# Kernel optimization log

Measured on AMD Instinct MI355X. Metric: run time of the kernel, lower is better.

## Reference

```python
import jax, jax.numpy as jnp
import numpy as np

B, L = 1024, 256
POOL, FM, HEAD, EMB = 4, 64, 64, 48  # input_size=256, pool_size=4 -> 64x64 maps


def _smooth(x, scale):
    # replicate-pad box filter of width 2*scale+1, via cumsum (single pass)
    w = 2 * scale + 1
    xp = jnp.pad(x, ((0, 0), (scale, scale)), mode='edge')          # (B, L+2s)
    c = jnp.pad(jnp.cumsum(xp, axis=1), ((0, 0), (1, 0)))           # (B, L+2s+1)
    return (c[:, w:] - c[:, :-w]) / w                               # (B, L)


def _picker(g, wmap, wbias, fcw, fcb):
    # g: (B, 256, 256) pairwise feature map
    b = g.shape[0]
    p = g.reshape(b, FM, POOL, FM, POOL).mean(axis=(2, 4))          # AvgPool2d(4): (B,64,64)
    h = jax.nn.elu(jnp.einsum('bij,hij->bh', p, wmap) + wbias)      # (B, head)
    return jax.nn.elu(h @ fcw.T + fcb)                              # (B, emb)


def setup_inputs() -> dict:
    key = jax.random.key(0)
    ks = jax.random.split(key, 16)
    x = jax.random.uniform(ks[0], (B, L), dtype=jnp.float32)
    d = {'x': x}
    for i, name in enumerate(['di', 'ndi', 'dd']):
        d[f'wm_{name}'] = jax.random.normal(ks[1 + 4 * i], (HEAD, FM, FM), jnp.float32)
        d[f'b_{name}'] = jax.random.normal(ks[2 + 4 * i], (HEAD,), jnp.float32)
        d[f'fcw_{name}'] = jax.random.normal(ks[3 + 4 * i], (EMB, HEAD), jnp.float32) * (1.0 / np.sqrt(HEAD))
        d[f'fcb_{name}'] = jax.random.normal(ks[4 + 4 * i], (EMB,), jnp.float32) * 0.01
    d['fc1_w'] = jax.random.normal(ks[13], (48, 3 * EMB), jnp.float32) * (1.0 / np.sqrt(3 * EMB))
    d['fc1_b'] = jax.random.normal(ks[14], (48,), jnp.float32) * 0.01
    d['fc2_w'] = jax.random.normal(ks[15], (20, 48), jnp.float32) * (1.0 / np.sqrt(48))
    d['fc2_b'] = jnp.zeros((20,), jnp.float32)
    return d


def reference(x, wm_di, b_di, fcw_di, fcb_di,
              wm_ndi, b_ndi, fcw_ndi, fcb_ndi,
              wm_dd, b_dd, fcw_dd, fcb_dd,
              fc1_w, fc1_b, fc2_w, fc2_b):
    sm = _smooth(x, 2)
    diff = jnp.diff(sm, axis=1, prepend=x[:, :1])                   # (B, L)
    xi, xj = x[:, :, None], x[:, None, :]
    DI = xj - xi                                                    # (B, L, L)
    NDI = DI / (xj + xi + 1e-5)
    DD = diff[:, None, :] - diff[:, :, None]
    e_di = _picker(DI, wm_di, b_di, fcw_di, fcb_di)
    e_ndi = _picker(NDI, wm_ndi, b_ndi, fcw_ndi, fcb_ndi)
    e_dd = _picker(DD, wm_dd, b_dd, fcw_dd, fcb_dd)
    emb = jnp.concatenate([e_di, e_ndi, e_dd], axis=1)              # (B, 144)
    emb = jax.nn.elu(emb @ fc1_w.T + fc1_b)
    return emb @ fc2_w.T + fc2_b                                    # (B, 20)
```

## Files before the change

kernel.cpp:

```cpp
#include <hip/hip_runtime.h>
#include <hip/hip_bf16.h>
#include <math.h>

typedef __attribute__((ext_vector_type(8))) short short8;
typedef __attribute__((ext_vector_type(4))) float floatx4;

#define WS_WREDT 0u
#define WS_WMAT  (1u << 20)

__device__ __forceinline__ float eluf(float v) {
  return v > 0.f ? v : __expf(v) - 1.f;
}

__device__ __forceinline__ unsigned short f2bf(float f) {
  __hip_bfloat16 h = __float2bfloat16(f);
  return *reinterpret_cast<unsigned short*>(&h);
}

__global__ __launch_bounds__(256) void prep_kernel(
    const float* __restrict__ wm_di,
    const float* __restrict__ wm_ndi,
    const float* __restrict__ wm_dd,
    char* __restrict__ ws) {
  __shared__ float sm[64 * 65];
  const int t = threadIdx.x;
  if (blockIdx.x < 128) {
    const int sel = blockIdx.x >> 6, h = blockIdx.x & 63;
    const float* w = (sel ? wm_dd : wm_di) + h * 4096;
#pragma unroll 4
    for (int i = 0; i < 16; ++i) {
      const int e = i * 256 + t;
      sm[(e >> 6) * 65 + (e & 63)] = w[e];
    }
    __syncthreads();
    if (t < 64) {
      float cs = 0.f, rs = 0.f;
#pragma unroll 8
      for (int I = 0; I < 64; ++I) {
        cs += sm[I * 65 + t];
        rs += sm[t * 65 + I];
      }
      ((float*)(ws + WS_WREDT))[sel * 4096 + t * 64 + h] = cs - rs;
    }
  } else {
    const int gid = (blockIdx.x - 128) * 256 + t;
    const int lane = (gid >> 3) & 63, kstep = (gid >> 9) & 63, n = gid >> 15;
    const int h = n * 16 + (lane & 15);
    const int k = kstep * 32 + ((lane >> 4) << 3) + (gid & 7);
    const int I = k >> 5, tt = k & 31;
    const int J = (I + 1 + tt) & 63;
    float v = 0.f;
    if (!(tt == 31 && I >= 32))
      v = 0.0625f * (wm_ndi[h * 4096 + I * 64 + J] - wm_ndi[h * 4096 + J * 64 + I]);
    ((__hip_bfloat16*)(ws + WS_WMAT))[gid] = __float2bfloat16(v);
  }
}

__global__ __launch_bounds__(1024, 8) void fused_kernel(
    const float* __restrict__ x,
    const float* __restrict__ b_di, const float* __restrict__ b_ndi,
    const float* __restrict__ b_dd,
    const float* __restrict__ fcw_di, const float* __restrict__ fcb_di,
    const float* __restrict__ fcw_ndi, const float* __restrict__ fcb_ndi,
    const float* __restrict__ fcw_dd, const float* __restrict__ fcb_dd,
    const float* __restrict__ fc1_w, const float* __restrict__ fc1_b,
    const float* __restrict__ fc2_w, const float* __restrict__ fc2_b,
    const char* __restrict__ ws,
    float* __restrict__ out) {
  __shared__ float xs[2][256];
  __shared__ __align__(16) unsigned short ldsA[2][2][2048];
  __shared__ float pxs[2][64], pds[2][64];
  __shared__ float hp[16][4][2][16];
  __shared__ float hh[3][2][64];
  __shared__ float emb_s[2][144];
  __shared__ float f1v_s[2][48];

  const int t = threadIdx.x;
  const int b0 = blockIdx.x * 2;
  const float* __restrict__ wredT = (const float*)(ws + WS_WREDT);
  const short* __restrict__ wmaT = (const short*)(ws + WS_WMAT);

  if (t < 512) xs[t >> 8][t & 255] = x[(b0 + (t >> 8)) * 256 + (t & 255)];
  __syncthreads();

  if (t < 128) {
    const int r = t >> 6, m = t & 63;
    const float* __restrict__ xr = xs[r];
    const int b4 = 4 * m;
    pxs[r][m] = 0.25f * (xr[b4] + xr[b4 + 1] + xr[b4 + 2] + xr[b4 + 3]);
    const int i3 = min(b4 + 4, 255), i4 = min(b4 + 5, 255);
    const float smv = 0.2f * (xr[b4 + 1] + xr[b4 + 2] + xr[b4 + 3] + xr[i3] + xr[i4]);
    float prev = __shfl_up(smv, 1, 64);
    if (m == 0) prev = xr[0];
    pds[r][m] = 0.25f * (smv - prev);
  }

#pragma unroll
  for (int i = 0; i < 4; ++i) {
    const int cc = t + i * 1024;
    const int r = cc >> 11, e = cc & 2047;
    const int I = e >> 5;
    const int J = (I + 1 + (e & 31)) & 63;
    const float4 xiv = *(const float4*)&xs[r][I << 2];
    const float4 xjv = *(const float4*)&xs[r][J << 2];
    const float xi_a[4] = {xiv.x, xiv.y, xiv.z, xiv.w};
    const float xj_a[4] = {xjv.x + 1e-5f, xjv.y + 1e-5f, xjv.z + 1e-5f, xjv.w + 1e-5f};
    const float xn_a[4] = {xjv.x, xjv.y, xjv.z, xjv.w};
    float s = 0.f;
#pragma unroll
    for (int a = 0; a < 4; ++a) {
#pragma unroll
      for (int c = 0; c < 4; ++c) {
        const float num = xn_a[c] - xi_a[a];
        const float den = xj_a[c] + xi_a[a];
        s += num * __builtin_amdgcn_rcpf(den);
      }
    }
    const unsigned short hi = f2bf(s);
    union { unsigned int u; float f; } hv; hv.u = ((unsigned int)hi) << 16;
    ldsA[0][r][e] = hi;
    ldsA[1][r][e] = f2bf(s - hv.f);
  }
  __syncthreads();

  {
    const int kh = t >> 6, lane = t & 63;
    const int arow = lane & 1;
    const int kofs = kh * 128 + ((lane >> 4) << 3);
#pragma unroll
    for (int n = 0; n < 4; ++n) {
      floatx4 acc = {0.f, 0.f, 0.f, 0.f};
#pragma unroll
      for (int s = 0; s < 4; ++s) {
        const int kk = kofs + s * 32;
        const short8 ah = *(const short8*)&ldsA[0][arow][kk];
        const short8 al = *(const short8*)&ldsA[1][arow][kk];
        const int kstep = kh * 4 + s;
        const short8 bv = *(const short8*)(wmaT + (((n * 64 + kstep) * 64 + lane) << 3));
        acc = __builtin_amdgcn_mfma_f32_16x16x32_bf16(ah, bv, acc, 0, 0, 0);
        acc = __builtin_amdgcn_mfma_f32_16x16x32_bf16(al, bv, acc, 0, 0, 0);
      }
      if (lane < 16) {
        hp[kh][n][0][lane] = acc[0];
        hp[kh][n][1][lane] = acc[1];
      }
    }
  }

  if (t < 128) {
    const int r = t >> 6, h = t & 63;
    float adi = b_di[h], add_ = b_dd[h];
#pragma unroll 8
    for (int K = 0; K < 64; ++K) {
      adi += pxs[r][K] * wredT[K * 64 + h];
      add_ += pds[r][K] * wredT[4096 + K * 64 + h];
    }
    hh[0][r][h] = eluf(adi);
    hh[2][r][h] = eluf(add_);
  }
  __syncthreads();

  if (t < 128) {
    const int row = t >> 6, h = t & 63;
    const int n = h >> 4, c = h & 15;
    float v = b_ndi[h];
#pragma unroll
    for (int kh = 0; kh < 16; ++kh) v += hp[kh][n][row][c];
    hh[1][row][h] = eluf(v);
  }
  __syncthreads();

  if (t < 2 * 144) {
    const int r = t / 144;
    const int k = t - r * 144;
    const int pick = k / 48;
    const int e = k - pick * 48;
    const float* __restrict__ fw = (pick == 0) ? fcw_di : (pick == 1) ? fcw_ndi : fcw_dd;
    const float* __restrict__ fb = (pick == 0) ? fcb_di : (pick == 1) ? fcb_ndi : fcb_dd;
    float a = fb[e];
#pragma unroll 8
    for (int hq = 0; hq < 64; ++hq) a += hh[pick][r][hq] * fw[e * 64 + hq];
    emb_s[r][k] = eluf(a);
  }
  __syncthreads();

  if (t < 2 * 48) {
    const int r = t / 48, o = t - (t / 48) * 48;
    float a = fc1_b[o];
#pragma unroll 8
    for (int k = 0; k < 144; ++k) a += emb_s[r][k] * fc1_w[o * 144 + k];
    f1v_s[r][o] = eluf(a);
  }
  __syncthreads();

  if (t < 2 * 20) {
    const int r = t / 20, o = t - (t / 20) * 20;
    float a = fc2_b[o];
#pragma unroll
    for (int j = 0; j < 48; ++j) a += f1v_s[r][j] * fc2_w[o * 48 + j];
    out[(b0 + r) * 20 + o] = a;
  }
}

extern "C" void kernel_launch(void* const* d_in, const int* in_sizes, int n_in,
                              void* d_out, int out_size, void* d_ws, size_t ws_size,
                              hipStream_t stream) {
  const float* x       = (const float*)d_in[0];
  const float* wm_di   = (const float*)d_in[1];
  const float* b_di    = (const float*)d_in[2];
  const float* fcw_di  = (const float*)d_in[3];
  const float* fcb_di  = (const float*)d_in[4];
  const float* wm_ndi  = (const float*)d_in[5];
  const float* b_ndi   = (const float*)d_in[6];
  const float* fcw_ndi = (const float*)d_in[7];
  const float* fcb_ndi = (const float*)d_in[8];
  const float* wm_dd   = (const float*)d_in[9];
  const float* b_dd    = (const float*)d_in[10];
  const float* fcw_dd  = (const float*)d_in[11];
  const float* fcb_dd  = (const float*)d_in[12];
  const float* fc1_w   = (const float*)d_in[13];
  const float* fc1_b   = (const float*)d_in[14];
  const float* fc2_w   = (const float*)d_in[15];
  const float* fc2_b   = (const float*)d_in[16];
  float* out = (float*)d_out;
  char* ws = (char*)d_ws;

  prep_kernel<<<640, 256, 0, stream>>>(wm_di, wm_ndi, wm_dd, ws);
  fused_kernel<<<512, 1024, 0, stream>>>(
      x, b_di, b_ndi, b_dd,
      fcw_di, fcb_di, fcw_ndi, fcb_ndi, fcw_dd, fcb_dd,
      fc1_w, fc1_b, fc2_w, fc2_b, ws, out);
}
```

Baseline: 27.95 us.

## Pair NDI reciprocals algebraically and stage NDI weight prep through LDS

```diff
diff --git a/kernel.cpp b/kernel.cpp
--- a/kernel.cpp
+++ b/kernel.cpp
@@ -43,16 +43,29 @@
       ((float*)(ws + WS_WREDT))[sel * 4096 + t * 64 + h] = cs - rs;
     }
   } else {
-    const int gid = (blockIdx.x - 128) * 256 + t;
-    const int lane = (gid >> 3) & 63, kstep = (gid >> 9) & 63, n = gid >> 15;
-    const int h = n * 16 + (lane & 15);
-    const int k = kstep * 32 + ((lane >> 4) << 3) + (gid & 7);
-    const int I = k >> 5, tt = k & 31;
-    const int J = (I + 1 + tt) & 63;
-    float v = 0.f;
-    if (!(tt == 31 && I >= 32))
-      v = 0.0625f * (wm_ndi[h * 4096 + I * 64 + J] - wm_ndi[h * 4096 + J * 64 + I]);
-    ((__hip_bfloat16*)(ws + WS_WMAT))[gid] = __float2bfloat16(v);
+    const int h = blockIdx.x - 128;
+    const float* w = wm_ndi + h * 4096;
+#pragma unroll 4
+    for (int i = 0; i < 16; ++i) {
+      const int e = i * 256 + t;
+      sm[(e >> 6) * 65 + (e & 63)] = w[e];
+    }
+    __syncthreads();
+    const int kstep = t >> 2, kc = t & 3;
+    const int lane = kc * 16 + (h & 15);
+    const int n = h >> 4;
+    short8 sv;
+#pragma unroll
+    for (int j = 0; j < 8; ++j) {
+      const int k = kstep * 32 + kc * 8 + j;
+      const int I = k >> 5, tt = k & 31;
+      const int J = (I + 1 + tt) & 63;
+      float v = 0.f;
+      if (!(tt == 31 && I >= 32))
+        v = 0.0625f * (sm[I * 65 + J] - sm[J * 65 + I]);
+      sv[j] = (short)f2bf(v);
+    }
+    *(short8*)((__hip_bfloat16*)(ws + WS_WMAT) + (((n * 64 + kstep) * 64 + lane) << 3)) = sv;
   }
 }
 
@@ -95,7 +108,7 @@
     pds[r][m] = 0.25f * (smv - prev);
   }
 
-#pragma unroll
+#pragma unroll 1
   for (int i = 0; i < 4; ++i) {
     const int cc = t + i * 1024;
     const int r = cc >> 11, e = cc & 2047;
@@ -103,21 +116,22 @@
     const int J = (I + 1 + (e & 31)) & 63;
     const float4 xiv = *(const float4*)&xs[r][I << 2];
     const float4 xjv = *(const float4*)&xs[r][J << 2];
-    const float xi_a[4] = {xiv.x, xiv.y, xiv.z, xiv.w};
-    const float xj_a[4] = {xjv.x + 1e-5f, xjv.y + 1e-5f, xjv.z + 1e-5f, xjv.w + 1e-5f};
-    const float xn_a[4] = {xjv.x, xjv.y, xjv.z, xjv.w};
+    const float P01 = 2.f * xjv.x * xjv.y + (xjv.x + xjv.y) * 1e-5f;
+    const float P23 = 2.f * xjv.z * xjv.w + (xjv.z + xjv.w) * 1e-5f;
+    const float ya[4] = {xiv.x, xiv.y, xiv.z, xiv.w};
     float s = 0.f;
 #pragma unroll
     for (int a = 0; a < 4; ++a) {
-#pragma unroll
-      for (int c = 0; c < 4; ++c) {
-        const float num = xn_a[c] - xi_a[a];
-        const float den = xj_a[c] + xi_a[a];
-        s += num * __builtin_amdgcn_rcpf(den);
-      }
+      const float y = ya[a];
+      const float u = y + 1e-5f;
+      const float G = 2.f * y * u;
+      const float D0 = (xjv.x + u) * (xjv.y + u);
+      const float D1 = (xjv.z + u) * (xjv.w + u);
+      s += (P01 - G) * __builtin_amdgcn_rcpf(D0);
+      s += (P23 - G) * __builtin_amdgcn_rcpf(D1);
     }
     const unsigned short hi = f2bf(s);
-    union { unsigned int u; float f; } hv; hv.u = ((unsigned int)hi) << 16;
+    union { unsigned int uu; float f; } hv; hv.uu = ((unsigned int)hi) << 16;
     ldsA[0][r][e] = hi;
     ldsA[1][r][e] = f2bf(s - hv.f);
   }
@@ -225,7 +239,7 @@
   float* out = (float*)d_out;
   char* ws = (char*)d_ws;
 
-  prep_kernel<<<640, 256, 0, stream>>>(wm_di, wm_ndi, wm_dd, ws);
+  prep_kernel<<<192, 256, 0, stream>>>(wm_di, wm_ndi, wm_dd, ws);
   fused_kernel<<<512, 1024, 0, stream>>>(
       x, b_di, b_ndi, b_dd,
       fcw_di, fcb_di, fcw_ndi, fcb_ndi, fcw_dd, fcb_dd,
```

After: 27.04 us. 3.3% less time.
